# Kernel optimization log

Hardware: AMD Instinct MI355X
Metric: run time of the kernel (lower is better)

## Reference

```python
import jax, jax.numpy as jnp
import numpy as np

N_CODES = 4096
DIM = 1280
N_TOKENS = 32768


def _l2norm(v, axis=-1, eps=1e-12):
    return v / jnp.maximum(jnp.linalg.norm(v, axis=axis, keepdims=True), eps)


def setup_inputs() -> dict:
    key = jax.random.key(0)
    kx, ke = jax.random.split(key)
    # inputs are L2-normalized vectors per the module's docstring
    x = _l2norm(jax.random.normal(kx, (N_TOKENS, DIM), dtype=jnp.float32))
    # codebook init: uniform(-1/n_codes, 1/n_codes) then L2-normalized (as in __init__)
    embed = jax.random.uniform(ke, (N_CODES, DIM), dtype=jnp.float32,
                               minval=-1.0 / N_CODES, maxval=1.0 / N_CODES)
    embed = _l2norm(embed)
    return {"x": x, "embed": embed}


def reference(x, embed):
    x_sq = jnp.sum(x * x, axis=1, keepdims=True)            # (N, 1)
    e_sq = jnp.sum(embed * embed, axis=1)[None, :]          # (1, K)
    dist = -(x_sq - 2.0 * (x @ embed.T) + e_sq)             # (N, K)
    indices = jnp.argmax(dist, axis=-1)                     # (N,)
    quantized = embed[indices]                              # gather (N, D)
    commit_loss = jnp.mean((x - quantized) ** 2)
    # straight-through estimator
    quantized_ste = x + jax.lax.stop_gradient(quantized - x)
    return quantized_ste, indices, commit_loss
```

## Files before the change

### kernel.cpp

```cpp
#include <hip/hip_runtime.h>
#include <hip/hip_bf16.h>

typedef int i32x4 __attribute__((ext_vector_type(4)));

#define N_TOKENS 32768
#define N_CODES 4096
#define DIM 1280
#define NT 20
#define BUFSZ 32768

__device__ __forceinline__ void load_lds16(const void* g, void* l) {
    __builtin_amdgcn_global_load_lds(
        (const __attribute__((address_space(1))) unsigned int*)g,
        (__attribute__((address_space(3))) unsigned int*)l,
        16, 0, 0);
}

__global__ __launch_bounds__(256) void quantize_i8_kernel(
    const float* __restrict__ src, signed char* __restrict__ dst,
    float* __restrict__ scale, int nrows)
{
    int row = blockIdx.x * 4 + (threadIdx.x >> 6);
    if (row >= nrows) return;
    int lane = threadIdx.x & 63;
    const float4* s4 = (const float4*)(src + (size_t)row * DIM);
    float4 v[5];
    float amax = 0.f;
    #pragma unroll
    for (int j = 0; j < 5; ++j) {
        v[j] = s4[j * 64 + lane];
        amax = fmaxf(amax, fmaxf(fmaxf(fabsf(v[j].x), fabsf(v[j].y)),
                                 fmaxf(fabsf(v[j].z), fabsf(v[j].w))));
    }
    #pragma unroll
    for (int d = 1; d < 64; d <<= 1) amax = fmaxf(amax, __shfl_xor(amax, d));
    amax = fmaxf(amax, 1e-20f);
    float inv = 127.0f / amax;
    int* d4 = (int*)(dst + (size_t)row * DIM);
    #pragma unroll
    for (int j = 0; j < 5; ++j) {
        int q0 = (int)rintf(v[j].x * inv), q1 = (int)rintf(v[j].y * inv);
        int q2 = (int)rintf(v[j].z * inv), q3 = (int)rintf(v[j].w * inv);
        d4[j * 64 + lane] = (q0 & 0xFF) | ((q1 & 0xFF) << 8) |
                            ((q2 & 0xFF) << 16) | ((q3 & 0xFF) << 24);
    }
    if (lane == 0) scale[row] = amax * (1.0f / 127.0f);
}

__global__ __launch_bounds__(1024, 4) void gemm_argmax_kernel(
    const signed char* __restrict__ Xq, const signed char* __restrict__ Eq,
    const float* __restrict__ sx, const float* __restrict__ se,
    unsigned* __restrict__ pkeys)
{
    __shared__ __align__(16) char lds[4 * BUFSZ];

    int bid = blockIdx.x;
    int swz = (bid & 7) * 256 + (bid >> 3);
    int cb0 = swz >> 7, rb = swz & 127;
    int row0 = rb << 8, col0 = cb0 << 8;

    int tid = threadIdx.x;
    int wid = tid >> 6, lane = tid & 63;
    int wm = wid >> 2, wn = wid & 3;
    int lr = lane & 15, g = lane >> 4;

    int slot = (((lr & 1) << 2) + g) ^ ((lr >> 1) & 7);
    int aoff = ((wm << 5) + (lr >> 1)) * 128 + slot * 16;
    int boff = 16384 + ((wn << 5) + (lr >> 1)) * 128 + slot * 16;

    i32x4 acc[4][4] = {};

    auto STAGE = [&](int t) {
        int base = (t & 3) * BUFSZ;
        int k0 = t << 6;
        int f = tid;
        int rp = f >> 3, c = f & 7;
        int cp = c ^ (rp & 7);
        int gr = (rp << 1) + (cp >> 2);
        int kc = k0 + ((cp & 3) << 4);
        load_lds16(Xq + (size_t)(row0 + gr) * DIM + kc, lds + base + (f << 4));
        load_lds16(Eq + (size_t)(col0 + gr) * DIM + kc, lds + base + 16384 + (f << 4));
    };

    auto COMPUTE = [&](int t) {
        int base = (t & 3) * BUFSZ;
        const char* pA = lds + base + aoff;
        const char* pB = lds + base + boff;
        i32x4 a[4], b[4];
        #pragma unroll
        for (int m = 0; m < 4; ++m) a[m] = *(const i32x4*)(pA + (m << 10));
        #pragma unroll
        for (int n = 0; n < 4; ++n) b[n] = *(const i32x4*)(pB + (n << 10));
        __builtin_amdgcn_s_setprio(1);
        #pragma unroll
        for (int m = 0; m < 4; ++m)
            #pragma unroll
            for (int n = 0; n < 4; ++n)
                acc[m][n] = __builtin_amdgcn_mfma_i32_16x16x64_i8(
                    a[m], b[n], acc[m][n], 0, 0, 0);
        __builtin_amdgcn_s_setprio(0);
    };

    STAGE(0); STAGE(1); STAGE(2);
    asm volatile("s_waitcnt vmcnt(4)" ::: "memory");
    __builtin_amdgcn_s_barrier();
    __builtin_amdgcn_sched_barrier(0);

    for (int t = 0; t < NT - 3; ++t) {
        STAGE(t + 3);
        COMPUTE(t);
        asm volatile("s_waitcnt vmcnt(4)" ::: "memory");
        __builtin_amdgcn_s_barrier();
        __builtin_amdgcn_sched_barrier(0);
    }
    COMPUTE(NT - 3);
    asm volatile("s_waitcnt vmcnt(2)" ::: "memory");
    __builtin_amdgcn_s_barrier();
    __builtin_amdgcn_sched_barrier(0);
    COMPUTE(NT - 2);
    asm volatile("s_waitcnt vmcnt(0)" ::: "memory");
    __builtin_amdgcn_s_barrier();
    __builtin_amdgcn_sched_barrier(0);
    COMPUTE(NT - 1);
    __syncthreads();

    float se_l[4];
    #pragma unroll
    for (int n = 0; n < 4; ++n)
        se_l[n] = se[col0 + (wn << 6) + (n << 4) + lr];

    uint2* lk2 = (uint2*)lds;
    #pragma unroll
    for (int m = 0; m < 4; ++m) {
        #pragma unroll
        for (int r = 0; r < 4; ++r) {
            int row = (wm << 6) + (m << 4) + (g << 2) + r;
            float fx = sx[row0 + row];
            unsigned b1 = 0, b2 = 0;
            #pragma unroll
            for (int n = 0; n < 4; ++n) {
                float s = (float)acc[m][n][r] * (fx * se_l[n]);
                int cib = ((wn & 1) << 6) + (n << 4) + lr;
                unsigned u = __float_as_uint(s);
                u = (u & 0x80000000u) ? ~u : (u | 0x80000000u);
                unsigned key = (u & 0xFFFFFF80u) | (unsigned)(127 - cib);
                if (key > b1) { b2 = b1; b1 = key; }
                else if (key > b2) b2 = key;
            }
            #pragma unroll
            for (int d = 1; d < 16; d <<= 1) {
                unsigned o1 = __shfl_xor(b1, d), o2 = __shfl_xor(b2, d);
                if (o1 > b1) { b2 = (b1 > o2) ? b1 : o2; b1 = o1; }
                else if (o1 > b2) b2 = o1;
            }
            if (lr == 0) {
                uint2 v; v.x = b1; v.y = b2;
                lk2[(row << 2) + wn] = v;
            }
        }
    }
    __syncthreads();
    if (tid < 512) {
        int row = tid >> 1, h = tid & 1;
        uint2 p0 = lk2[(row << 2) + (h << 1)];
        uint2 p1 = lk2[(row << 2) + (h << 1) + 1];
        unsigned b1 = p0.x, b2 = p0.y;
        if (p1.x > b1) { b2 = (b1 > p1.y) ? b1 : p1.y; b1 = p1.x; }
        else if (p1.x > b2) b2 = p1.x;
        uint2 out; out.x = b1; out.y = b2;
        *(uint2*)&pkeys[((size_t)(row0 + row) << 6) + (((cb0 << 1) + h) << 1)] = out;
    }
}

__global__ __launch_bounds__(64) void refine_gather_kernel(
    const float* __restrict__ X, const float* __restrict__ E,
    const unsigned* __restrict__ pkeys, float* __restrict__ outq,
    float* __restrict__ outidx, float* __restrict__ sums)
{
    int token = blockIdx.x;
    int lane = threadIdx.x;
    unsigned k = pkeys[((size_t)token << 6) + lane];
    unsigned m = k & 0xFFFFFF80u;
    float s = __uint_as_float((m & 0x80000000u) ? (m & 0x7FFFFFFFu) : ~m);
    float smax = s;
    #pragma unroll
    for (int d = 1; d < 64; d <<= 1) smax = fmaxf(smax, __shfl_xor(smax, d));
    bool cand = s >= smax - 3e-3f;
    unsigned long long ball = __ballot(cand);

    const float4* x4 = (const float4*)(X + (size_t)token * DIM);
    float4 xv[5];
    #pragma unroll
    for (int j = 0; j < 5; ++j) xv[j] = x4[j * 64 + lane];

    double best_s = -1.0e300;
    int best_i = 0x7FFFFFFF;
    while (ball) {
        int src = __ffsll(ball) - 1;
        ball &= ball - 1;
        unsigned ck = __shfl(k, src);
        int cidx = ((src >> 1) << 7) + (127 - (int)(ck & 127u));
        const float4* e4 = (const float4*)(E + (size_t)cidx * DIM);
        double d = 0.0, ee = 0.0;
        #pragma unroll
        for (int j = 0; j < 5; ++j) {
            float4 ev = e4[j * 64 + lane];
            d += (double)xv[j].x * (double)ev.x + (double)xv[j].y * (double)ev.y
               + (double)xv[j].z * (double)ev.z + (double)xv[j].w * (double)ev.w;
            ee += (double)ev.x * (double)ev.x + (double)ev.y * (double)ev.y
                + (double)ev.z * (double)ev.z + (double)ev.w * (double)ev.w;
        }
        #pragma unroll
        for (int dd = 1; dd < 64; dd <<= 1) {
            d += __shfl_xor(d, dd);
            ee += __shfl_xor(ee, dd);
        }
        double sc = 2.0 * d - ee;
        if (sc > best_s || (sc == best_s && cidx < best_i)) { best_s = sc; best_i = cidx; }
    }

    const float4* e4 = (const float4*)(E + (size_t)best_i * DIM);
    float4* o4 = (float4*)(outq + (size_t)token * DIM);
    float local = 0.0f;
    #pragma unroll
    for (int j = 0; j < 5; ++j) {
        float4 q = e4[j * 64 + lane];
        o4[j * 64 + lane] = q;
        float dx = xv[j].x - q.x, dy = xv[j].y - q.y;
        float dz = xv[j].z - q.z, dw = xv[j].w - q.w;
        local += dx * dx + dy * dy + dz * dz + dw * dw;
    }
    #pragma unroll
    for (int d = 1; d < 64; d <<= 1) local += __shfl_xor(local, d);
    if (lane == 0) {
        sums[token] = local;
        outidx[token] = (float)best_i;
    }
}

__global__ __launch_bounds__(256) void loss_kernel(
    const float* __restrict__ sums, float* __restrict__ out_loss)
{
    __shared__ double red[256];
    int t = threadIdx.x;
    double s = 0.0;
    for (int i = t; i < N_TOKENS; i += 256) s += (double)sums[i];
    red[t] = s;
    __syncthreads();
    for (int off = 128; off > 0; off >>= 1) {
        if (t < off) red[t] += red[t + off];
        __syncthreads();
    }
    if (t == 0) out_loss[0] = (float)(red[0] / (double)((size_t)N_TOKENS * DIM));
}

extern "C" void kernel_launch(void* const* d_in, const int* in_sizes, int n_in,
                              void* d_out, int out_size, void* d_ws, size_t ws_size,
                              hipStream_t stream)
{
    const float* X = (const float*)d_in[0];
    const float* E = (const float*)d_in[1];

    float* outq = (float*)d_out;
    float* outidx = outq + (size_t)N_TOKENS * DIM;
    float* outloss = outidx + N_TOKENS;

    signed char* Xq = (signed char*)d_out;
    signed char* Eq = Xq + (size_t)N_TOKENS * DIM;
    float* sxs = (float*)(Eq + (size_t)N_CODES * DIM);
    float* ses = sxs + N_TOKENS;

    unsigned* pkeys = (unsigned*)d_ws;
    float* sums = (float*)((char*)d_ws + (size_t)N_TOKENS * 64 * sizeof(unsigned));

    quantize_i8_kernel<<<dim3(N_TOKENS / 4), dim3(256), 0, stream>>>(X, Xq, sxs, N_TOKENS);
    quantize_i8_kernel<<<dim3(N_CODES / 4), dim3(256), 0, stream>>>(E, Eq, ses, N_CODES);
    gemm_argmax_kernel<<<dim3(2048), dim3(1024), 0, stream>>>(Xq, Eq, sxs, ses, pkeys);
    refine_gather_kernel<<<dim3(N_TOKENS), dim3(64), 0, stream>>>(X, E, pkeys, outq, outidx, sums);
    loss_kernel<<<dim3(1), dim3(256), 0, stream>>>(sums, outloss);
}
```

Before: 380.6 us.

## Merge quantize launches, remap GEMM tiles per XCD, double-step pipeline, skip single-candidate refine

Fuses the two int8 quantize launches into one grid covering both tokens and codes, which saves a launch. Changes the block-to-tile mapping so each XCD owns two code column blocks and sweeps row blocks, aiming for better L2 reuse of the codebook. Restructures the GEMM main loop to compute two K-stages and then issue two stage loads between barriers, with four stages prefetched up front. The refine kernel now skips the fp64 rescoring when only one candidate survives the threshold. The new barrier placement and vmcnt counts change how much load latency is overlapped, which risks less overlap or a stall in the pipeline.

```diff
diff --git a/kernel.cpp b/kernel.cpp
--- a/kernel.cpp
+++ b/kernel.cpp
@@ -17,13 +17,23 @@
 }
 
 __global__ __launch_bounds__(256) void quantize_i8_kernel(
-    const float* __restrict__ src, signed char* __restrict__ dst,
-    float* __restrict__ scale, int nrows)
+    const float* __restrict__ X, const float* __restrict__ E,
+    signed char* __restrict__ Xq, signed char* __restrict__ Eq,
+    float* __restrict__ sxs, float* __restrict__ ses)
 {
     int row = blockIdx.x * 4 + (threadIdx.x >> 6);
-    if (row >= nrows) return;
+    const float* src;
+    signed char* dst;
+    float* scale;
+    if (row < N_TOKENS) {
+        src = X + (size_t)row * DIM; dst = Xq + (size_t)row * DIM; scale = sxs + row;
+    } else {
+        int r = row - N_TOKENS;
+        if (r >= N_CODES) return;
+        src = E + (size_t)r * DIM; dst = Eq + (size_t)r * DIM; scale = ses + r;
+    }
     int lane = threadIdx.x & 63;
-    const float4* s4 = (const float4*)(src + (size_t)row * DIM);
+    const float4* s4 = (const float4*)src;
     float4 v[5];
     float amax = 0.f;
     #pragma unroll
@@ -36,7 +46,7 @@
     for (int d = 1; d < 64; d <<= 1) amax = fmaxf(amax, __shfl_xor(amax, d));
     amax = fmaxf(amax, 1e-20f);
     float inv = 127.0f / amax;
-    int* d4 = (int*)(dst + (size_t)row * DIM);
+    int* d4 = (int*)dst;
     #pragma unroll
     for (int j = 0; j < 5; ++j) {
         int q0 = (int)rintf(v[j].x * inv), q1 = (int)rintf(v[j].y * inv);
@@ -44,7 +54,7 @@
         d4[j * 64 + lane] = (q0 & 0xFF) | ((q1 & 0xFF) << 8) |
                             ((q2 & 0xFF) << 16) | ((q3 & 0xFF) << 24);
     }
-    if (lane == 0) scale[row] = amax * (1.0f / 127.0f);
+    if (lane == 0) *scale = amax * (1.0f / 127.0f);
 }
 
 __global__ __launch_bounds__(1024, 4) void gemm_argmax_kernel(
@@ -55,8 +65,9 @@
     __shared__ __align__(16) char lds[4 * BUFSZ];
 
     int bid = blockIdx.x;
-    int swz = (bid & 7) * 256 + (bid >> 3);
-    int cb0 = swz >> 7, rb = swz & 127;
+    int xcd = bid & 7, i = bid >> 3;
+    int cb0 = (xcd << 1) + (i & 1);
+    int rb = i >> 1;
     int row0 = rb << 8, col0 = cb0 << 8;
 
     int tid = threadIdx.x;
@@ -101,27 +112,31 @@
         __builtin_amdgcn_s_setprio(0);
     };
 
-    STAGE(0); STAGE(1); STAGE(2);
+    STAGE(0); STAGE(1); STAGE(2); STAGE(3);
     asm volatile("s_waitcnt vmcnt(4)" ::: "memory");
     __builtin_amdgcn_s_barrier();
     __builtin_amdgcn_sched_barrier(0);
 
-    for (int t = 0; t < NT - 3; ++t) {
-        STAGE(t + 3);
+    #pragma unroll 1
+    for (int s = 0; s < 8; ++s) {
+        int t = s * 2;
         COMPUTE(t);
+        COMPUTE(t + 1);
+        __builtin_amdgcn_s_barrier();
+        __builtin_amdgcn_sched_barrier(0);
+        STAGE(t + 4);
+        STAGE(t + 5);
         asm volatile("s_waitcnt vmcnt(4)" ::: "memory");
         __builtin_amdgcn_s_barrier();
         __builtin_amdgcn_sched_barrier(0);
     }
-    COMPUTE(NT - 3);
-    asm volatile("s_waitcnt vmcnt(2)" ::: "memory");
-    __builtin_amdgcn_s_barrier();
-    __builtin_amdgcn_sched_barrier(0);
-    COMPUTE(NT - 2);
+    COMPUTE(16);
+    COMPUTE(17);
     asm volatile("s_waitcnt vmcnt(0)" ::: "memory");
     __builtin_amdgcn_s_barrier();
     __builtin_amdgcn_sched_barrier(0);
-    COMPUTE(NT - 1);
+    COMPUTE(18);
+    COMPUTE(19);
     __syncthreads();
 
     float se_l[4];
@@ -193,30 +208,37 @@
     #pragma unroll
     for (int j = 0; j < 5; ++j) xv[j] = x4[j * 64 + lane];
 
-    double best_s = -1.0e300;
-    int best_i = 0x7FFFFFFF;
-    while (ball) {
+    int best_i;
+    if (__popcll(ball) == 1) {
         int src = __ffsll(ball) - 1;
-        ball &= ball - 1;
         unsigned ck = __shfl(k, src);
-        int cidx = ((src >> 1) << 7) + (127 - (int)(ck & 127u));
-        const float4* e4 = (const float4*)(E + (size_t)cidx * DIM);
-        double d = 0.0, ee = 0.0;
-        #pragma unroll
-        for (int j = 0; j < 5; ++j) {
-            float4 ev = e4[j * 64 + lane];
-            d += (double)xv[j].x * (double)ev.x + (double)xv[j].y * (double)ev.y
-               + (double)xv[j].z * (double)ev.z + (double)xv[j].w * (double)ev.w;
-            ee += (double)ev.x * (double)ev.x + (double)ev.y * (double)ev.y
-                + (double)ev.z * (double)ev.z + (double)ev.w * (double)ev.w;
+        best_i = ((src >> 1) << 7) + (127 - (int)(ck & 127u));
+    } else {
+        double best_s = -1.0e300;
+        best_i = 0x7FFFFFFF;
+        while (ball) {
+            int src = __ffsll(ball) - 1;
+            ball &= ball - 1;
+            unsigned ck = __shfl(k, src);
+            int cidx = ((src >> 1) << 7) + (127 - (int)(ck & 127u));
+            const float4* e4 = (const float4*)(E + (size_t)cidx * DIM);
+            double d = 0.0, ee = 0.0;
+            #pragma unroll
+            for (int j = 0; j < 5; ++j) {
+                float4 ev = e4[j * 64 + lane];
+                d += (double)xv[j].x * (double)ev.x + (double)xv[j].y * (double)ev.y
+                   + (double)xv[j].z * (double)ev.z + (double)xv[j].w * (double)ev.w;
+                ee += (double)ev.x * (double)ev.x + (double)ev.y * (double)ev.y
+                    + (double)ev.z * (double)ev.z + (double)ev.w * (double)ev.w;
+            }
+            #pragma unroll
+            for (int dd = 1; dd < 64; dd <<= 1) {
+                d += __shfl_xor(d, dd);
+                ee += __shfl_xor(ee, dd);
+            }
+            double sc = 2.0 * d - ee;
+            if (sc > best_s || (sc == best_s && cidx < best_i)) { best_s = sc; best_i = cidx; }
         }
-        #pragma unroll
-        for (int dd = 1; dd < 64; dd <<= 1) {
-            d += __shfl_xor(d, dd);
-            ee += __shfl_xor(ee, dd);
-        }
-        double sc = 2.0 * d - ee;
-        if (sc > best_s || (sc == best_s && cidx < best_i)) { best_s = sc; best_i = cidx; }
     }
 
     const float4* e4 = (const float4*)(E + (size_t)best_i * DIM);
@@ -273,8 +295,8 @@
     unsigned* pkeys = (unsigned*)d_ws;
     float* sums = (float*)((char*)d_ws + (size_t)N_TOKENS * 64 * sizeof(unsigned));
 
-    quantize_i8_kernel<<<dim3(N_TOKENS / 4), dim3(256), 0, stream>>>(X, Xq, sxs, N_TOKENS);
-    quantize_i8_kernel<<<dim3(N_CODES / 4), dim3(256), 0, stream>>>(E, Eq, ses, N_CODES);
+    quantize_i8_kernel<<<dim3((N_TOKENS + N_CODES) / 4), dim3(256), 0, stream>>>(
+        X, E, Xq, Eq, sxs, ses);
     gemm_argmax_kernel<<<dim3(2048), dim3(1024), 0, stream>>>(Xq, Eq, sxs, ses, pkeys);
     refine_gather_kernel<<<dim3(N_TOKENS), dim3(64), 0, stream>>>(X, E, pkeys, outq, outidx, sums);
     loss_kernel<<<dim3(1), dim3(256), 0, stream>>>(sums, outloss);
```

Result: slower. 391.9 us (+3.0%).
